# Optimization experiments

Measured on AMD Instinct MI355X. Metric: run time of the kernel, lower is better.

## Reference

```python
import jax, jax.numpy as jnp
import numpy as np

N = 100000   # nodes
E = 1600000  # edges (before self loops)
IN, HID, OUT = 128, 128, 64


def setup_inputs() -> dict:
    key = jax.random.key(0)
    ks = jax.random.split(key, 5)
    x = jax.random.normal(ks[0], (N, IN), dtype=jnp.float32)
    edge_index = jax.random.randint(ks[1], (2, E), 0, N, dtype=jnp.int32)
    W1 = jax.random.normal(ks[2], (IN, HID), dtype=jnp.float32) * (1.0 / np.sqrt(IN))
    b1 = jnp.zeros((HID,), dtype=jnp.float32)
    W2 = jax.random.normal(ks[3], (HID, OUT), dtype=jnp.float32) * (1.0 / np.sqrt(HID))
    b2 = jnp.zeros((OUT,), dtype=jnp.float32)
    return {"x": x, "edge_index": edge_index, "W1": W1, "b1": b1, "W2": W2, "b2": b2}


def _gcn_conv(x, W, b, src, dst, norm):
    # linear transform first (small GEMM), then normalized scatter-add aggregation
    h = x @ W                                   # [N, d_out]
    msg = h[src] * norm[:, None]                # [E+N, d_out] gathered messages
    agg = jax.ops.segment_sum(msg, dst, num_segments=N)
    return agg + b


def reference(x, edge_index, W1, b1, W2, b2):
    loops = jnp.arange(N, dtype=edge_index.dtype)
    src = jnp.concatenate([edge_index[0], loops])   # add self loops (PyG GCNConv default)
    dst = jnp.concatenate([edge_index[1], loops])
    # symmetric normalization D^{-1/2} (A+I) D^{-1/2}
    deg = jax.ops.segment_sum(jnp.ones_like(dst, dtype=x.dtype), dst, num_segments=N)
    dinv = jnp.where(deg > 0, jax.lax.rsqrt(deg), 0.0)
    norm = dinv[src] * dinv[dst]                # [E+N]

    h = _gcn_conv(x, W1, b1, src, dst, norm)
    h = jax.nn.relu(h)
    out = _gcn_conv(h, W2, b2, src, dst, norm)
    return out
```

## Files before the change

kernel.cpp:

```cpp
#include <hip/hip_runtime.h>
#include <hip/hip_bf16.h>

#define IN_DIM  128
#define HID_DIM 128
#define OUT_DIM 64

typedef unsigned short ushort_t;
struct ushort4_t { ushort_t x, y, z, w; };
typedef __attribute__((ext_vector_type(8))) short bf16x8;
typedef __attribute__((ext_vector_type(4))) float f32x4;

__device__ __forceinline__ float bf2f(ushort_t u) {
    return __uint_as_float(((unsigned int)u) << 16);
}
__device__ __forceinline__ short f2bf_s(float v) {
    __hip_bfloat16 t = __float2bfloat16(v);
    return *(short*)&t;
}
__device__ __forceinline__ unsigned int pack2(float a, float b) {
    return ((unsigned int)(ushort_t)f2bf_s(b) << 16) | (ushort_t)f2bf_s(a);
}

__global__ __launch_bounds__(256, 2) void fused_gemm1_count(
        const float* __restrict__ x, const float* __restrict__ W,
        unsigned int* __restrict__ h,
        const int* __restrict__ dst, int* __restrict__ cnt, int* __restrict__ rank,
        int N, int E, int NT) {
    const int bid = blockIdx.x;
    const int tid = threadIdx.x;

    if (bid & 1) {
        const int lane = tid & 63;
        const int m    = lane & 15;
        const int quad = lane >> 4;
        const int gw   = (bid >> 1) * 4 + (tid >> 6);
        const int NW   = 1024;

        bf16x8 a[8][4];
        #pragma unroll
        for (int ct = 0; ct < 8; ++ct)
            #pragma unroll
            for (int kc = 0; kc < 4; ++kc)
                #pragma unroll
                for (int j = 0; j < 8; ++j)
                    a[ct][kc][j] = f2bf_s(W[(size_t)(kc * 32 + quad * 8 + j) * HID_DIM + ct * 16 + m]);

        for (int t = gw; t < NT; t += NW) {
            const int n0 = t * 16;
            int node = n0 + m; if (node >= N) node = N - 1;
            const float* xr = x + (size_t)node * IN_DIM + quad * 8;
            f32x4 acc[8];
            #pragma unroll
            for (int ct = 0; ct < 8; ++ct) acc[ct] = (f32x4){0.f, 0.f, 0.f, 0.f};
            #pragma unroll
            for (int kc = 0; kc < 4; ++kc) {
                const float4 v0 = *(const float4*)(xr + kc * 32);
                const float4 v1 = *(const float4*)(xr + kc * 32 + 4);
                bf16x8 b;
                b[0] = f2bf_s(v0.x); b[1] = f2bf_s(v0.y); b[2] = f2bf_s(v0.z); b[3] = f2bf_s(v0.w);
                b[4] = f2bf_s(v1.x); b[5] = f2bf_s(v1.y); b[6] = f2bf_s(v1.z); b[7] = f2bf_s(v1.w);
                #pragma unroll
                for (int ct = 0; ct < 8; ++ct)
                    acc[ct] = __builtin_amdgcn_mfma_f32_16x16x32_bf16(a[ct][kc], b, acc[ct], 0, 0, 0);
            }
            if (n0 + m < N) {
                unsigned int* o = h + (size_t)(n0 + m) * (HID_DIM / 2) + quad * 2;
                #pragma unroll
                for (int ct = 0; ct < 8; ++ct) {
                    uint2 pv;
                    pv.x = pack2(acc[ct][0], acc[ct][1]);
                    pv.y = pack2(acc[ct][2], acc[ct][3]);
                    *(uint2*)(o + ct * 8) = pv;
                }
            }
        }
    } else {
        const int ct = (bid >> 1) * 256 + tid;
        const int CT = 256 * 256;
        const int nq = E >> 2;
        const int4* d4 = (const int4*)dst;
        for (int q = ct; q < nq; q += CT) {
            const int4 d = d4[q];
            int4 r;
            r.x = atomicAdd(&cnt[d.x], 1);
            r.y = atomicAdd(&cnt[d.y], 1);
            r.z = atomicAdd(&cnt[d.z], 1);
            r.w = atomicAdd(&cnt[d.w], 1);
            ((int4*)rank)[q] = r;
        }
        for (int e = (nq << 2) + ct; e < E; e += CT)
            rank[e] = atomicAdd(&cnt[dst[e]], 1);
    }
}

__global__ void scan_partial(const int* __restrict__ cnt, int* __restrict__ bsum,
                             float* __restrict__ dinv, int N) {
    __shared__ int wsum[4];
    const int t = threadIdx.x;
    const int base = blockIdx.x * 2048 + t * 8;
    int s = 0;
    #pragma unroll
    for (int i = 0; i < 8; ++i) {
        if (base + i < N) {
            const int c = cnt[base + i];
            dinv[base + i] = rsqrtf((float)(c + 1));
            s += (c + 3) & ~3;
        }
    }
    #pragma unroll
    for (int off = 32; off > 0; off >>= 1) s += __shfl_down(s, off);
    const int lane = t & 63, w = t >> 6;
    if (lane == 0) wsum[w] = s;
    __syncthreads();
    if (t == 0) bsum[blockIdx.x] = wsum[0] + wsum[1] + wsum[2] + wsum[3];
}

__global__ void scan_partials(int* __restrict__ bsum, int S) {
    const int t = threadIdx.x;
    int running = 0;
    for (int base = 0; base < S; base += 64) {
        int i = base + t;
        int v = (i < S) ? bsum[i] : 0;
        int incl = v;
        #pragma unroll
        for (int off = 1; off < 64; off <<= 1) {
            int u = __shfl_up(incl, off);
            if (t >= off) incl += u;
        }
        if (i < S) bsum[i] = running + incl - v;
        running += __shfl(incl, 63);
    }
}

__global__ void scan_write(const int* __restrict__ cnt, const int* __restrict__ bsum,
                           int* __restrict__ row_start, int N) {
    __shared__ int wsum[4];
    const int t = threadIdx.x;
    const int base = blockIdx.x * 2048 + t * 8;
    int v[8];
    #pragma unroll
    for (int i = 0; i < 8; ++i) v[i] = (base + i < N) ? ((cnt[base + i] + 3) & ~3) : 0;
    int s = v[0] + v[1] + v[2] + v[3] + v[4] + v[5] + v[6] + v[7];
    const int lane = t & 63, w = t >> 6;
    int incl = s;
    #pragma unroll
    for (int off = 1; off < 64; off <<= 1) {
        int u = __shfl_up(incl, off);
        if (lane >= off) incl += u;
    }
    if (lane == 63) wsum[w] = incl;
    __syncthreads();
    int woff = 0;
    for (int i = 0; i < w; ++i) woff += wsum[i];
    int run = bsum[blockIdx.x] + woff + (incl - s);
    #pragma unroll
    for (int i = 0; i < 8; ++i) {
        if (base + i < N) row_start[base + i] = run;
        run += v[i];
    }
}

__global__ void fill_pack4(const int* __restrict__ src, const int* __restrict__ dst,
                           const int* __restrict__ rank, const int* __restrict__ row_start,
                           const float* __restrict__ dinv, int E, int2* __restrict__ pack) {
    const int q = blockIdx.x * blockDim.x + threadIdx.x;
    const int nq = E >> 2;
    if (q < nq) {
        const int4 s = ((const int4*)src)[q];
        const int4 d = ((const int4*)dst)[q];
        const int4 r = ((const int4*)rank)[q];
        int2 p;
        p.x = s.x; p.y = __float_as_int(dinv[s.x] * dinv[d.x]);
        pack[row_start[d.x] + r.x] = p;
        p.x = s.y; p.y = __float_as_int(dinv[s.y] * dinv[d.y]);
        pack[row_start[d.y] + r.y] = p;
        p.x = s.z; p.y = __float_as_int(dinv[s.z] * dinv[d.z]);
        pack[row_start[d.z] + r.z] = p;
        p.x = s.w; p.y = __float_as_int(dinv[s.w] * dinv[d.w]);
        pack[row_start[d.w] + r.w] = p;
    }
    if (q == 0) {
        for (int e = nq << 2; e < E; ++e) {
            int2 p;
            p.x = src[e]; p.y = __float_as_int(dinv[src[e]] * dinv[dst[e]]);
            pack[row_start[dst[e]] + rank[e]] = p;
        }
    }
}

__global__ __launch_bounds__(256) void gemm2_mfma(
        const ushort_t* __restrict__ agg, const float* __restrict__ b1,
        const float* __restrict__ W2, unsigned int* __restrict__ h2,
        int N, int NT, int NW) {
    const int tid  = threadIdx.x;
    const int lane = tid & 63;
    const int m    = lane & 15;
    const int quad = lane >> 4;
    const int gw   = blockIdx.x * 4 + (tid >> 6);

    bf16x8 a[4][4];
    #pragma unroll
    for (int ct = 0; ct < 4; ++ct)
        #pragma unroll
        for (int kc = 0; kc < 4; ++kc)
            #pragma unroll
            for (int j = 0; j < 8; ++j)
                a[ct][kc][j] = f2bf_s(W2[(size_t)(kc * 32 + quad * 8 + j) * OUT_DIM + ct * 16 + m]);

    float4 b1v[8];
    #pragma unroll
    for (int kc = 0; kc < 4; ++kc) {
        b1v[kc * 2]     = *(const float4*)(b1 + kc * 32 + quad * 8);
        b1v[kc * 2 + 1] = *(const float4*)(b1 + kc * 32 + quad * 8 + 4);
    }

    for (int t = gw; t < NT; t += NW) {
        const int n0 = t * 16;
        int node = n0 + m; if (node >= N) node = N - 1;
        const ushort_t* ar = agg + (size_t)node * HID_DIM + quad * 8;
        f32x4 acc[4];
        #pragma unroll
        for (int ct = 0; ct < 4; ++ct) acc[ct] = (f32x4){0.f, 0.f, 0.f, 0.f};
        #pragma unroll
        for (int kc = 0; kc < 4; ++kc) {
            const ushort4_t r0 = *(const ushort4_t*)(ar + kc * 32);
            const ushort4_t r1 = *(const ushort4_t*)(ar + kc * 32 + 4);
            const float4 ba = b1v[kc * 2], bb = b1v[kc * 2 + 1];
            bf16x8 b;
            b[0] = f2bf_s(fmaxf(bf2f(r0.x) + ba.x, 0.f));
            b[1] = f2bf_s(fmaxf(bf2f(r0.y) + ba.y, 0.f));
            b[2] = f2bf_s(fmaxf(bf2f(r0.z) + ba.z, 0.f));
            b[3] = f2bf_s(fmaxf(bf2f(r0.w) + ba.w, 0.f));
            b[4] = f2bf_s(fmaxf(bf2f(r1.x) + bb.x, 0.f));
            b[5] = f2bf_s(fmaxf(bf2f(r1.y) + bb.y, 0.f));
            b[6] = f2bf_s(fmaxf(bf2f(r1.z) + bb.z, 0.f));
            b[7] = f2bf_s(fmaxf(bf2f(r1.w) + bb.w, 0.f));
            #pragma unroll
            for (int ct = 0; ct < 4; ++ct)
                acc[ct] = __builtin_amdgcn_mfma_f32_16x16x32_bf16(a[ct][kc], b, acc[ct], 0, 0, 0);
        }
        if (n0 + m < N) {
            unsigned int* o = h2 + (size_t)(n0 + m) * (OUT_DIM / 2) + quad * 2;
            #pragma unroll
            for (int ct = 0; ct < 4; ++ct) {
                uint2 pv;
                pv.x = pack2(acc[ct][0], acc[ct][1]);
                pv.y = pack2(acc[ct][2], acc[ct][3]);
                *(uint2*)(o + ct * 8) = pv;
            }
        }
    }
}

template<int D, bool BF16_OUT>
__global__ void gather_bf16(const ushort_t* __restrict__ h, const int2* __restrict__ pack,
                            const int* __restrict__ row_start, const int* __restrict__ cnt,
                            const float* __restrict__ dinv, const float* __restrict__ bias,
                            int N, void* __restrict__ outv) {
    const int TPN = D / 4;
    const int NPB = 256 / TPN;
    const int t = threadIdx.x;
    const int node = blockIdx.x * NPB + t / TPN;
    if (node >= N) return;
    const int f = (t & (TPN - 1)) * 4;
    const float dd = dinv[node];

    const ushort4_t self = *(const ushort4_t*)(h + (size_t)node * D + f);
    const float sn = dd * dd;
    float4 acc;
    acc.x = bf2f(self.x) * sn; acc.y = bf2f(self.y) * sn;
    acc.z = bf2f(self.z) * sn; acc.w = bf2f(self.w) * sn;
    if (bias) {
        const float4 b = *(const float4*)(bias + f);
        acc.x += b.x; acc.y += b.y; acc.z += b.z; acc.w += b.w;
    }

    const int2* pk = pack + row_start[node];
    const int cpad = (cnt[node] + 3) & ~3;
    for (int e = 0; e < cpad; e += 4) {
        const int4 a = *(const int4*)(pk + e);
        const int4 b = *(const int4*)(pk + e + 2);
        {
            const ushort4_t v = *(const ushort4_t*)(h + (size_t)a.x * D + f);
            const float n = __int_as_float(a.y);
            acc.x += bf2f(v.x) * n; acc.y += bf2f(v.y) * n;
            acc.z += bf2f(v.z) * n; acc.w += bf2f(v.w) * n;
        }
        {
            const ushort4_t v = *(const ushort4_t*)(h + (size_t)a.z * D + f);
            const float n = __int_as_float(a.w);
            acc.x += bf2f(v.x) * n; acc.y += bf2f(v.y) * n;
            acc.z += bf2f(v.z) * n; acc.w += bf2f(v.w) * n;
        }
        {
            const ushort4_t v = *(const ushort4_t*)(h + (size_t)b.x * D + f);
            const float n = __int_as_float(b.y);
            acc.x += bf2f(v.x) * n; acc.y += bf2f(v.y) * n;
            acc.z += bf2f(v.z) * n; acc.w += bf2f(v.w) * n;
        }
        {
            const ushort4_t v = *(const ushort4_t*)(h + (size_t)b.z * D + f);
            const float n = __int_as_float(b.w);
            acc.x += bf2f(v.x) * n; acc.y += bf2f(v.y) * n;
            acc.z += bf2f(v.z) * n; acc.w += bf2f(v.w) * n;
        }
    }
    if (BF16_OUT) {
        unsigned int* out = (unsigned int*)outv;
        uint2 pv;
        pv.x = pack2(acc.x, acc.y);
        pv.y = pack2(acc.z, acc.w);
        *(uint2*)(out + ((size_t)node * D + f) / 2) = pv;
    } else {
        float* out = (float*)outv;
        *(float4*)(out + (size_t)node * D + f) = acc;
    }
}

extern "C" void kernel_launch(void* const* d_in, const int* in_sizes, int n_in,
                              void* d_out, int out_size, void* d_ws, size_t ws_size,
                              hipStream_t stream) {
    const float* x   = (const float*)d_in[0];
    const int*   ei  = (const int*)  d_in[1];
    const float* W1  = (const float*)d_in[2];
    const float* b1  = (const float*)d_in[3];
    const float* W2  = (const float*)d_in[4];
    const float* b2  = (const float*)d_in[5];
    float* out = (float*)d_out;

    const int N = in_sizes[0] / IN_DIM;
    const int E = in_sizes[1] / 2;
    const int* src = ei;
    const int* dst = ei + E;

    const int PACK_CAP = E + 4 * N;
    float* dinv      = (float*)d_ws;
    int*   cnt       = (int*)(dinv + N);
    int*   row_start = cnt + N;
    int*   bsum      = row_start + N;
    size_t off       = (size_t)(3 * N + 1024);
    off = (off + 3) & ~(size_t)3;
    int2*  pack      = (int2*)((int*)d_ws + off);
    unsigned int* h1 = (unsigned int*)(pack + PACK_CAP);
    unsigned int* agg1 = h1 + (size_t)N * (HID_DIM / 2);
    int*   rank      = (int*)agg1;
    unsigned int* h2 = h1;

    const int B = 256;
    const int S = (N + 2047) / 2048;
    const int NT = (N + 15) / 16;

    hipMemsetAsync(cnt, 0, (size_t)N * sizeof(int), stream);
    hipMemsetAsync(pack, 0, (size_t)PACK_CAP * sizeof(int2), stream);
    fused_gemm1_count<<<512, 256, 0, stream>>>(x, W1, h1, dst, cnt, rank, N, E, NT);

    scan_partial<<<S, 256, 0, stream>>>(cnt, bsum, dinv, N);
    scan_partials<<<1, 64, 0, stream>>>(bsum, S);
    scan_write<<<S, 256, 0, stream>>>(cnt, bsum, row_start, N);

    fill_pack4<<<((E >> 2) + B - 1) / B, B, 0, stream>>>(src, dst, rank, row_start, dinv, E, pack);

    gather_bf16<HID_DIM, true><<<(N + 7) / 8, 256, 0, stream>>>(
        (const ushort_t*)h1, pack, row_start, cnt, dinv, nullptr, N, (void*)agg1);

    gemm2_mfma<<<768, 256, 0, stream>>>(
        (const ushort_t*)agg1, b1, W2, h2, N, NT, 768 * 4);

    gather_bf16<OUT_DIM, false><<<(N + 15) / 16, 256, 0, stream>>>(
        (const ushort_t*)h2, pack, row_start, cnt, dinv, b2, N, (void*)out);
}
```

Measured before the change: 316.4 us.

## Shrink CSR pack to source-only ints and fold scan, bias, relu into neighbors

The packed edge array now holds only the source index (4 bytes instead of 8), and the edge norm is recomputed in the gather from dinv[src]*dinv[dst]. Padding slots are marked -1 in scan_write, so the large pack memset goes away. The separate single-block scan_partials launch is removed, and each scan_write block now sums the preceding block totals itself. Bias and ReLU move from gemm2's input stage into the first gather's epilogue, so gemm2 loads bf16 vectors directly. Together this cuts edge-list traffic, one memset and one launch, at the cost of an extra dinv gather per edge and a redundant prefix sum in every scan block.

```diff
diff --git a/kernel.cpp b/kernel.cpp
--- a/kernel.cpp
+++ b/kernel.cpp
@@ -115,31 +115,25 @@
     if (t == 0) bsum[blockIdx.x] = wsum[0] + wsum[1] + wsum[2] + wsum[3];
 }
 
-__global__ void scan_partials(int* __restrict__ bsum, int S) {
+__global__ void scan_write(const int* __restrict__ cnt, const int* __restrict__ bsum,
+                           int* __restrict__ row_start, int* __restrict__ pack, int N) {
+    __shared__ int wsum[4];
+    __shared__ int blockoff;
     const int t = threadIdx.x;
-    int running = 0;
-    for (int base = 0; base < S; base += 64) {
-        int i = base + t;
-        int v = (i < S) ? bsum[i] : 0;
-        int incl = v;
-        #pragma unroll
-        for (int off = 1; off < 64; off <<= 1) {
-            int u = __shfl_up(incl, off);
-            if (t >= off) incl += u;
-        }
-        if (i < S) bsum[i] = running + incl - v;
-        running += __shfl(incl, 63);
-    }
-}
-
-__global__ void scan_write(const int* __restrict__ cnt, const int* __restrict__ bsum,
-                           int* __restrict__ row_start, int N) {
-    __shared__ int wsum[4];
-    const int t = threadIdx.x;
+    if (t < 64) {
+        int a = 0;
+        for (int idx = t; idx < blockIdx.x; idx += 64) a += bsum[idx];
+        #pragma unroll
+        for (int off = 32; off > 0; off >>= 1) a += __shfl_down(a, off);
+        if (t == 0) blockoff = a;
+    }
     const int base = blockIdx.x * 2048 + t * 8;
-    int v[8];
-    #pragma unroll
-    for (int i = 0; i < 8; ++i) v[i] = (base + i < N) ? ((cnt[base + i] + 3) & ~3) : 0;
+    int c[8], v[8];
+    #pragma unroll
+    for (int i = 0; i < 8; ++i) {
+        c[i] = (base + i < N) ? cnt[base + i] : 0;
+        v[i] = (c[i] + 3) & ~3;
+    }
     int s = v[0] + v[1] + v[2] + v[3] + v[4] + v[5] + v[6] + v[7];
     const int lane = t & 63, w = t >> 6;
     int incl = s;
@@ -152,44 +146,39 @@
     __syncthreads();
     int woff = 0;
     for (int i = 0; i < w; ++i) woff += wsum[i];
-    int run = bsum[blockIdx.x] + woff + (incl - s);
+    int run = blockoff + woff + (incl - s);
     #pragma unroll
     for (int i = 0; i < 8; ++i) {
-        if (base + i < N) row_start[base + i] = run;
-        run += v[i];
+        if (base + i < N) {
+            row_start[base + i] = run;
+            for (int p = c[i]; p < v[i]; ++p) pack[run + p] = -1;
+            run += v[i];
+        }
     }
 }
 
 __global__ void fill_pack4(const int* __restrict__ src, const int* __restrict__ dst,
                            const int* __restrict__ rank, const int* __restrict__ row_start,
-                           const float* __restrict__ dinv, int E, int2* __restrict__ pack) {
+                           int E, int* __restrict__ pack) {
     const int q = blockIdx.x * blockDim.x + threadIdx.x;
     const int nq = E >> 2;
     if (q < nq) {
         const int4 s = ((const int4*)src)[q];
         const int4 d = ((const int4*)dst)[q];
         const int4 r = ((const int4*)rank)[q];
-        int2 p;
-        p.x = s.x; p.y = __float_as_int(dinv[s.x] * dinv[d.x]);
-        pack[row_start[d.x] + r.x] = p;
-        p.x = s.y; p.y = __float_as_int(dinv[s.y] * dinv[d.y]);
-        pack[row_start[d.y] + r.y] = p;
-        p.x = s.z; p.y = __float_as_int(dinv[s.z] * dinv[d.z]);
-        pack[row_start[d.z] + r.z] = p;
-        p.x = s.w; p.y = __float_as_int(dinv[s.w] * dinv[d.w]);
-        pack[row_start[d.w] + r.w] = p;
+        pack[row_start[d.x] + r.x] = s.x;
+        pack[row_start[d.y] + r.y] = s.y;
+        pack[row_start[d.z] + r.z] = s.z;
+        pack[row_start[d.w] + r.w] = s.w;
     }
     if (q == 0) {
-        for (int e = nq << 2; e < E; ++e) {
-            int2 p;
-            p.x = src[e]; p.y = __float_as_int(dinv[src[e]] * dinv[dst[e]]);
-            pack[row_start[dst[e]] + rank[e]] = p;
-        }
+        for (int e = nq << 2; e < E; ++e)
+            pack[row_start[dst[e]] + rank[e]] = src[e];
     }
 }
 
 __global__ __launch_bounds__(256) void gemm2_mfma(
-        const ushort_t* __restrict__ agg, const float* __restrict__ b1,
+        const ushort_t* __restrict__ agg,
         const float* __restrict__ W2, unsigned int* __restrict__ h2,
         int N, int NT, int NW) {
     const int tid  = threadIdx.x;
@@ -207,13 +196,6 @@
             for (int j = 0; j < 8; ++j)
                 a[ct][kc][j] = f2bf_s(W2[(size_t)(kc * 32 + quad * 8 + j) * OUT_DIM + ct * 16 + m]);
 
-    float4 b1v[8];
-    #pragma unroll
-    for (int kc = 0; kc < 4; ++kc) {
-        b1v[kc * 2]     = *(const float4*)(b1 + kc * 32 + quad * 8);
-        b1v[kc * 2 + 1] = *(const float4*)(b1 + kc * 32 + quad * 8 + 4);
-    }
-
     for (int t = gw; t < NT; t += NW) {
         const int n0 = t * 16;
         int node = n0 + m; if (node >= N) node = N - 1;
@@ -223,18 +205,7 @@
         for (int ct = 0; ct < 4; ++ct) acc[ct] = (f32x4){0.f, 0.f, 0.f, 0.f};
         #pragma unroll
         for (int kc = 0; kc < 4; ++kc) {
-            const ushort4_t r0 = *(const ushort4_t*)(ar + kc * 32);
-            const ushort4_t r1 = *(const ushort4_t*)(ar + kc * 32 + 4);
-            const float4 ba = b1v[kc * 2], bb = b1v[kc * 2 + 1];
-            bf16x8 b;
-            b[0] = f2bf_s(fmaxf(bf2f(r0.x) + ba.x, 0.f));
-            b[1] = f2bf_s(fmaxf(bf2f(r0.y) + ba.y, 0.f));
-            b[2] = f2bf_s(fmaxf(bf2f(r0.z) + ba.z, 0.f));
-            b[3] = f2bf_s(fmaxf(bf2f(r0.w) + ba.w, 0.f));
-            b[4] = f2bf_s(fmaxf(bf2f(r1.x) + bb.x, 0.f));
-            b[5] = f2bf_s(fmaxf(bf2f(r1.y) + bb.y, 0.f));
-            b[6] = f2bf_s(fmaxf(bf2f(r1.z) + bb.z, 0.f));
-            b[7] = f2bf_s(fmaxf(bf2f(r1.w) + bb.w, 0.f));
+            const bf16x8 b = *(const bf16x8*)(ar + kc * 32);
             #pragma unroll
             for (int ct = 0; ct < 4; ++ct)
                 acc[ct] = __builtin_amdgcn_mfma_f32_16x16x32_bf16(a[ct][kc], b, acc[ct], 0, 0, 0);
@@ -252,8 +223,8 @@
     }
 }
 
-template<int D, bool BF16_OUT>
-__global__ void gather_bf16(const ushort_t* __restrict__ h, const int2* __restrict__ pack,
+template<int D, bool BF16_OUT, bool RELU>
+__global__ void gather_bf16(const ushort_t* __restrict__ h, const int* __restrict__ pack,
                             const int* __restrict__ row_start, const int* __restrict__ cnt,
                             const float* __restrict__ dinv, const float* __restrict__ bias,
                             int N, void* __restrict__ outv) {
@@ -270,40 +241,37 @@
     float4 acc;
     acc.x = bf2f(self.x) * sn; acc.y = bf2f(self.y) * sn;
     acc.z = bf2f(self.z) * sn; acc.w = bf2f(self.w) * sn;
-    if (bias) {
-        const float4 b = *(const float4*)(bias + f);
-        acc.x += b.x; acc.y += b.y; acc.z += b.z; acc.w += b.w;
-    }
-
-    const int2* pk = pack + row_start[node];
+    const float4 bv = *(const float4*)(bias + f);
+    acc.x += bv.x; acc.y += bv.y; acc.z += bv.z; acc.w += bv.w;
+
+    const int* pk = pack + row_start[node];
     const int cpad = (cnt[node] + 3) & ~3;
     for (int e = 0; e < cpad; e += 4) {
-        const int4 a = *(const int4*)(pk + e);
-        const int4 b = *(const int4*)(pk + e + 2);
-        {
-            const ushort4_t v = *(const ushort4_t*)(h + (size_t)a.x * D + f);
-            const float n = __int_as_float(a.y);
-            acc.x += bf2f(v.x) * n; acc.y += bf2f(v.y) * n;
-            acc.z += bf2f(v.z) * n; acc.w += bf2f(v.w) * n;
-        }
-        {
-            const ushort4_t v = *(const ushort4_t*)(h + (size_t)a.z * D + f);
-            const float n = __int_as_float(a.w);
-            acc.x += bf2f(v.x) * n; acc.y += bf2f(v.y) * n;
-            acc.z += bf2f(v.z) * n; acc.w += bf2f(v.w) * n;
-        }
-        {
-            const ushort4_t v = *(const ushort4_t*)(h + (size_t)b.x * D + f);
-            const float n = __int_as_float(b.y);
-            acc.x += bf2f(v.x) * n; acc.y += bf2f(v.y) * n;
-            acc.z += bf2f(v.z) * n; acc.w += bf2f(v.w) * n;
-        }
-        {
-            const ushort4_t v = *(const ushort4_t*)(h + (size_t)b.z * D + f);
-            const float n = __int_as_float(b.w);
-            acc.x += bf2f(v.x) * n; acc.y += bf2f(v.y) * n;
-            acc.z += bf2f(v.z) * n; acc.w += bf2f(v.w) * n;
-        }
+        const int4 s4 = *(const int4*)(pk + e);
+        const int i0 = s4.x < 0 ? 0 : s4.x;
+        const int i1 = s4.y < 0 ? 0 : s4.y;
+        const int i2 = s4.z < 0 ? 0 : s4.z;
+        const int i3 = s4.w < 0 ? 0 : s4.w;
+        const float n0 = s4.x < 0 ? 0.f : dinv[i0] * dd;
+        const float n1 = s4.y < 0 ? 0.f : dinv[i1] * dd;
+        const float n2 = s4.z < 0 ? 0.f : dinv[i2] * dd;
+        const float n3 = s4.w < 0 ? 0.f : dinv[i3] * dd;
+        const ushort4_t v0 = *(const ushort4_t*)(h + (size_t)i0 * D + f);
+        const ushort4_t v1 = *(const ushort4_t*)(h + (size_t)i1 * D + f);
+        const ushort4_t v2 = *(const ushort4_t*)(h + (size_t)i2 * D + f);
+        const ushort4_t v3 = *(const ushort4_t*)(h + (size_t)i3 * D + f);
+        acc.x += bf2f(v0.x) * n0; acc.y += bf2f(v0.y) * n0;
+        acc.z += bf2f(v0.z) * n0; acc.w += bf2f(v0.w) * n0;
+        acc.x += bf2f(v1.x) * n1; acc.y += bf2f(v1.y) * n1;
+        acc.z += bf2f(v1.z) * n1; acc.w += bf2f(v1.w) * n1;
+        acc.x += bf2f(v2.x) * n2; acc.y += bf2f(v2.y) * n2;
+        acc.z += bf2f(v2.z) * n2; acc.w += bf2f(v2.w) * n2;
+        acc.x += bf2f(v3.x) * n3; acc.y += bf2f(v3.y) * n3;
+        acc.z += bf2f(v3.z) * n3; acc.w += bf2f(v3.w) * n3;
+    }
+    if (RELU) {
+        acc.x = fmaxf(acc.x, 0.f); acc.y = fmaxf(acc.y, 0.f);
+        acc.z = fmaxf(acc.z, 0.f); acc.w = fmaxf(acc.w, 0.f);
     }
     if (BF16_OUT) {
         unsigned int* out = (unsigned int*)outv;
@@ -340,7 +308,7 @@
     int*   bsum      = row_start + N;
     size_t off       = (size_t)(3 * N + 1024);
     off = (off + 3) & ~(size_t)3;
-    int2*  pack      = (int2*)((int*)d_ws + off);
+    int*   pack      = (int*)d_ws + off;
     unsigned int* h1 = (unsigned int*)(pack + PACK_CAP);
     unsigned int* agg1 = h1 + (size_t)N * (HID_DIM / 2);
     int*   rank      = (int*)agg1;
@@ -351,21 +319,19 @@
     const int NT = (N + 15) / 16;
 
     hipMemsetAsync(cnt, 0, (size_t)N * sizeof(int), stream);
-    hipMemsetAsync(pack, 0, (size_t)PACK_CAP * sizeof(int2), stream);
     fused_gemm1_count<<<512, 256, 0, stream>>>(x, W1, h1, dst, cnt, rank, N, E, NT);
 
     scan_partial<<<S, 256, 0, stream>>>(cnt, bsum, dinv, N);
-    scan_partials<<<1, 64, 0, stream>>>(bsum, S);
-    scan_write<<<S, 256, 0, stream>>>(cnt, bsum, row_start, N);
-
-    fill_pack4<<<((E >> 2) + B - 1) / B, B, 0, stream>>>(src, dst, rank, row_start, dinv, E, pack);
-
-    gather_bf16<HID_DIM, true><<<(N + 7) / 8, 256, 0, stream>>>(
-        (const ushort_t*)h1, pack, row_start, cnt, dinv, nullptr, N, (void*)agg1);
+    scan_write<<<S, 256, 0, stream>>>(cnt, bsum, row_start, pack, N);
+
+    fill_pack4<<<((E >> 2) + B - 1) / B, B, 0, stream>>>(src, dst, rank, row_start, E, pack);
+
+    gather_bf16<HID_DIM, true, true><<<(N + 7) / 8, 256, 0, stream>>>(
+        (const ushort_t*)h1, pack, row_start, cnt, dinv, b1, N, (void*)agg1);
 
     gemm2_mfma<<<768, 256, 0, stream>>>(
-        (const ushort_t*)agg1, b1, W2, h2, N, NT, 768 * 4);
-
-    gather_bf16<OUT_DIM, false><<<(N + 15) / 16, 256, 0, stream>>>(
+        (const ushort_t*)agg1, W2, h2, N, NT, 768 * 4);
+
+    gather_bf16<OUT_DIM, false, false><<<(N + 15) / 16, 256, 0, stream>>>(
         (const ushort_t*)h2, pack, row_start, cnt, dinv, b2, N, (void*)out);
 }
```

New measurement: 353.5 us. +11.7%, slower.

## Drop pack memset, fold block-offset scan into scan_write, move bias+ReLU to gather

Applied to the files above, without the earlier changes.

Removes the full memset of the padded edge-pack buffer and instead zeroes only the padding slots of each row inside scan_write. It also removes the single-block scan_partials launch: each scan_write block sums the preceding block totals itself. Bias and ReLU for layer 1 move into the first gather's epilogue, so gemm2 loads bf16x8 operands directly with no per-element convert. Cost: scan_write blocks redundantly read the prefix of bsum, and padding writes are scattered.

```diff
diff --git a/kernel.cpp b/kernel.cpp
--- a/kernel.cpp
+++ b/kernel.cpp
@@ -115,31 +115,25 @@
     if (t == 0) bsum[blockIdx.x] = wsum[0] + wsum[1] + wsum[2] + wsum[3];
 }
 
-__global__ void scan_partials(int* __restrict__ bsum, int S) {
+__global__ void scan_write(const int* __restrict__ cnt, const int* __restrict__ bsum,
+                           int* __restrict__ row_start, int2* __restrict__ pack, int N) {
+    __shared__ int wsum[4];
+    __shared__ int blockoff;
     const int t = threadIdx.x;
-    int running = 0;
-    for (int base = 0; base < S; base += 64) {
-        int i = base + t;
-        int v = (i < S) ? bsum[i] : 0;
-        int incl = v;
-        #pragma unroll
-        for (int off = 1; off < 64; off <<= 1) {
-            int u = __shfl_up(incl, off);
-            if (t >= off) incl += u;
-        }
-        if (i < S) bsum[i] = running + incl - v;
-        running += __shfl(incl, 63);
-    }
-}
-
-__global__ void scan_write(const int* __restrict__ cnt, const int* __restrict__ bsum,
-                           int* __restrict__ row_start, int N) {
-    __shared__ int wsum[4];
-    const int t = threadIdx.x;
+    if (t < 64) {
+        int a = 0;
+        for (int idx = t; idx < blockIdx.x; idx += 64) a += bsum[idx];
+        #pragma unroll
+        for (int off = 32; off > 0; off >>= 1) a += __shfl_down(a, off);
+        if (t == 0) blockoff = a;
+    }
     const int base = blockIdx.x * 2048 + t * 8;
-    int v[8];
-    #pragma unroll
-    for (int i = 0; i < 8; ++i) v[i] = (base + i < N) ? ((cnt[base + i] + 3) & ~3) : 0;
+    int c[8], v[8];
+    #pragma unroll
+    for (int i = 0; i < 8; ++i) {
+        c[i] = (base + i < N) ? cnt[base + i] : 0;
+        v[i] = (c[i] + 3) & ~3;
+    }
     int s = v[0] + v[1] + v[2] + v[3] + v[4] + v[5] + v[6] + v[7];
     const int lane = t & 63, w = t >> 6;
     int incl = s;
@@ -152,11 +146,15 @@
     __syncthreads();
     int woff = 0;
     for (int i = 0; i < w; ++i) woff += wsum[i];
-    int run = bsum[blockIdx.x] + woff + (incl - s);
+    int run = blockoff + woff + (incl - s);
+    const int2 zr = {0, 0};
     #pragma unroll
     for (int i = 0; i < 8; ++i) {
-        if (base + i < N) row_start[base + i] = run;
-        run += v[i];
+        if (base + i < N) {
+            row_start[base + i] = run;
+            for (int p = c[i]; p < v[i]; ++p) pack[run + p] = zr;
+            run += v[i];
+        }
     }
 }
 
@@ -189,7 +187,7 @@
 }
 
 __global__ __launch_bounds__(256) void gemm2_mfma(
-        const ushort_t* __restrict__ agg, const float* __restrict__ b1,
+        const ushort_t* __restrict__ agg,
         const float* __restrict__ W2, unsigned int* __restrict__ h2,
         int N, int NT, int NW) {
     const int tid  = threadIdx.x;
@@ -207,13 +205,6 @@
             for (int j = 0; j < 8; ++j)
                 a[ct][kc][j] = f2bf_s(W2[(size_t)(kc * 32 + quad * 8 + j) * OUT_DIM + ct * 16 + m]);
 
-    float4 b1v[8];
-    #pragma unroll
-    for (int kc = 0; kc < 4; ++kc) {
-        b1v[kc * 2]     = *(const float4*)(b1 + kc * 32 + quad * 8);
-        b1v[kc * 2 + 1] = *(const float4*)(b1 + kc * 32 + quad * 8 + 4);
-    }
-
     for (int t = gw; t < NT; t += NW) {
         const int n0 = t * 16;
         int node = n0 + m; if (node >= N) node = N - 1;
@@ -223,18 +214,7 @@
         for (int ct = 0; ct < 4; ++ct) acc[ct] = (f32x4){0.f, 0.f, 0.f, 0.f};
         #pragma unroll
         for (int kc = 0; kc < 4; ++kc) {
-            const ushort4_t r0 = *(const ushort4_t*)(ar + kc * 32);
-            const ushort4_t r1 = *(const ushort4_t*)(ar + kc * 32 + 4);
-            const float4 ba = b1v[kc * 2], bb = b1v[kc * 2 + 1];
-            bf16x8 b;
-            b[0] = f2bf_s(fmaxf(bf2f(r0.x) + ba.x, 0.f));
-            b[1] = f2bf_s(fmaxf(bf2f(r0.y) + ba.y, 0.f));
-            b[2] = f2bf_s(fmaxf(bf2f(r0.z) + ba.z, 0.f));
-            b[3] = f2bf_s(fmaxf(bf2f(r0.w) + ba.w, 0.f));
-            b[4] = f2bf_s(fmaxf(bf2f(r1.x) + bb.x, 0.f));
-            b[5] = f2bf_s(fmaxf(bf2f(r1.y) + bb.y, 0.f));
-            b[6] = f2bf_s(fmaxf(bf2f(r1.z) + bb.z, 0.f));
-            b[7] = f2bf_s(fmaxf(bf2f(r1.w) + bb.w, 0.f));
+            const bf16x8 b = *(const bf16x8*)(ar + kc * 32);
             #pragma unroll
             for (int ct = 0; ct < 4; ++ct)
                 acc[ct] = __builtin_amdgcn_mfma_f32_16x16x32_bf16(a[ct][kc], b, acc[ct], 0, 0, 0);
@@ -252,7 +232,7 @@
     }
 }
 
-template<int D, bool BF16_OUT>
+template<int D, bool BF16_OUT, bool RELU>
 __global__ void gather_bf16(const ushort_t* __restrict__ h, const int2* __restrict__ pack,
                             const int* __restrict__ row_start, const int* __restrict__ cnt,
                             const float* __restrict__ dinv, const float* __restrict__ bias,
@@ -270,10 +250,8 @@
     float4 acc;
     acc.x = bf2f(self.x) * sn; acc.y = bf2f(self.y) * sn;
     acc.z = bf2f(self.z) * sn; acc.w = bf2f(self.w) * sn;
-    if (bias) {
-        const float4 b = *(const float4*)(bias + f);
-        acc.x += b.x; acc.y += b.y; acc.z += b.z; acc.w += b.w;
-    }
+    const float4 bv = *(const float4*)(bias + f);
+    acc.x += bv.x; acc.y += bv.y; acc.z += bv.z; acc.w += bv.w;
 
     const int2* pk = pack + row_start[node];
     const int cpad = (cnt[node] + 3) & ~3;
@@ -304,6 +282,10 @@
             acc.x += bf2f(v.x) * n; acc.y += bf2f(v.y) * n;
             acc.z += bf2f(v.z) * n; acc.w += bf2f(v.w) * n;
         }
+    }
+    if (RELU) {
+        acc.x = fmaxf(acc.x, 0.f); acc.y = fmaxf(acc.y, 0.f);
+        acc.z = fmaxf(acc.z, 0.f); acc.w = fmaxf(acc.w, 0.f);
     }
     if (BF16_OUT) {
         unsigned int* out = (unsigned int*)outv;
@@ -351,21 +333,19 @@
     const int NT = (N + 15) / 16;
 
     hipMemsetAsync(cnt, 0, (size_t)N * sizeof(int), stream);
-    hipMemsetAsync(pack, 0, (size_t)PACK_CAP * sizeof(int2), stream);
     fused_gemm1_count<<<512, 256, 0, stream>>>(x, W1, h1, dst, cnt, rank, N, E, NT);
 
     scan_partial<<<S, 256, 0, stream>>>(cnt, bsum, dinv, N);
-    scan_partials<<<1, 64, 0, stream>>>(bsum, S);
-    scan_write<<<S, 256, 0, stream>>>(cnt, bsum, row_start, N);
+    scan_write<<<S, 256, 0, stream>>>(cnt, bsum, row_start, pack, N);
 
     fill_pack4<<<((E >> 2) + B - 1) / B, B, 0, stream>>>(src, dst, rank, row_start, dinv, E, pack);
 
-    gather_bf16<HID_DIM, true><<<(N + 7) / 8, 256, 0, stream>>>(
-        (const ushort_t*)h1, pack, row_start, cnt, dinv, nullptr, N, (void*)agg1);
+    gather_bf16<HID_DIM, true, true><<<(N + 7) / 8, 256, 0, stream>>>(
+        (const ushort_t*)h1, pack, row_start, cnt, dinv, b1, N, (void*)agg1);
 
     gemm2_mfma<<<768, 256, 0, stream>>>(
-        (const ushort_t*)agg1, b1, W2, h2, N, NT, 768 * 4);
-
-    gather_bf16<OUT_DIM, false><<<(N + 15) / 16, 256, 0, stream>>>(
+        (const ushort_t*)agg1, W2, h2, N, NT, 768 * 4);
+
+    gather_bf16<OUT_DIM, false, false><<<(N + 15) / 16, 256, 0, stream>>>(
         (const ushort_t*)h2, pack, row_start, cnt, dinv, b2, N, (void*)out);
 }
```

Measured after the change: 312.2 us. No clear change (-1.3%).
